# Kernel tuning notes

Hardware: AMD Instinct MI355X
Metric: run time of the kernel (lower is better)

Reference implementation:

```python
import jax, jax.numpy as jnp
import numpy as np

B, T, D, H = 2, 2048, 1024, 16
HD = D // H  # head_size = 64
EPS = 1e-5


def _layernorm(x, g, b):
    mu = jnp.mean(x, axis=-1, keepdims=True)
    var = jnp.mean(jnp.square(x - mu), axis=-1, keepdims=True)
    return (x - mu) * jax.lax.rsqrt(var + EPS) * g + b


def setup_inputs() -> dict:
    key = jax.random.key(0)
    ks = jax.random.split(key, 16)
    s = 0.02
    return {
        "x": jax.random.normal(ks[0], (B, T, D), jnp.float32),
        # per-head Q/K/V linears, stacked over heads: [H, D, HD] (in,out layout)
        "wq": jax.random.normal(ks[1], (H, D, HD), jnp.float32) * s,
        "bq": jnp.zeros((H, HD), jnp.float32),
        "wk": jax.random.normal(ks[2], (H, D, HD), jnp.float32) * s,
        "bk": jnp.zeros((H, HD), jnp.float32),
        "wv": jax.random.normal(ks[3], (H, D, HD), jnp.float32) * s,
        "bv": jnp.zeros((H, HD), jnp.float32),
        "wp": jax.random.normal(ks[4], (D, D), jnp.float32) * s,
        "bp": jnp.zeros((D,), jnp.float32),
        "w1": jax.random.normal(ks[5], (D, 4 * D), jnp.float32) * s,
        "b1": jnp.zeros((4 * D,), jnp.float32),
        "w2": jax.random.normal(ks[6], (4 * D, D), jnp.float32) * s,
        "b2": jnp.zeros((D,), jnp.float32),
        "ln1_g": jnp.ones((D,), jnp.float32),
        "ln1_b": jnp.zeros((D,), jnp.float32),
        "lnf_g": jnp.ones((D,), jnp.float32),
        "lnf_b": jnp.zeros((D,), jnp.float32),
        "ln2_g": jnp.ones((D,), jnp.float32),
        "ln2_b": jnp.zeros((D,), jnp.float32),
    }


def reference(x, wq, bq, wk, bk, wv, bv, wp, bp, w1, b1, w2, b2,
              ln1_g, ln1_b, lnf_g, lnf_b, ln2_g, ln2_b):
    b_, t_, d_ = x.shape
    # batched per-head projections: [B,H,T,HD]
    Q = jnp.einsum('btd,hde->bhte', x, wq) + bq[None, :, None, :]
    K = jnp.einsum('btd,hde->bhte', x, wk) + bk[None, :, None, :]
    V = jnp.einsum('btd,hde->bhte', x, wv) + bv[None, :, None, :]
    # raw attention scores, scaled -- NOTE: no softmax, no mask (matches source)
    wei = jnp.einsum('bhte,bhse->bhts', Q, K) * (HD ** -0.5)
    attn = jnp.einsum('bhts,bhse->bhte', wei, V)  # [B,H,T,HD]
    # concat heads along last dim == [B,T,H*HD]
    cat = attn.transpose(0, 2, 1, 3).reshape(b_, t_, d_)
    Kc = K.transpose(0, 2, 1, 3).reshape(b_, t_, d_)
    Vc = V.transpose(0, 2, 1, 3).reshape(b_, t_, d_)
    out = cat @ wp + bp
    out1 = _layernorm(x + out, ln1_g, ln1_b)
    # FeedForward: ln(idx + net(idx)) internally
    ff = jax.nn.relu(out1 @ w1 + b1) @ w2 + b2
    ffo = _layernorm(out1 + ff, lnf_g, lnf_b)
    out2 = _layernorm(out1 + ffo, ln2_g, ln2_b)
    return (out2, Kc, Vc)
```

## Files before the change

kernel.cpp:

```cpp
#include <hip/hip_runtime.h>

typedef unsigned short u16;
typedef __attribute__((ext_vector_type(4))) float f32x4;
typedef __attribute__((ext_vector_type(8))) __bf16 bf16x8;
typedef __attribute__((ext_vector_type(8))) unsigned short u16x8;
typedef __attribute__((ext_vector_type(4))) unsigned short u16x4;

__device__ __forceinline__ u16 f2b(float f) {
    unsigned int u = __builtin_bit_cast(unsigned int, f);
    u = (u + 0x7FFFu + ((u >> 16) & 1u)) >> 16;
    return (u16)u;
}
__device__ __forceinline__ float b2f(u16 h) {
    unsigned int u = ((unsigned int)h) << 16;
    return __builtin_bit_cast(float, u);
}

__device__ __forceinline__ void gload_lds16(const u16* g, u16* l) {
    __builtin_amdgcn_global_load_lds(
        (const __attribute__((address_space(1))) void*)g,
        (__attribute__((address_space(3))) void*)l,
        16, 0, 0);
}

__device__ __forceinline__ bf16x8 lds_frag(const u16* p) {
    u16x8 t = *(const u16x8*)p;
    return __builtin_bit_cast(bf16x8, t);
}

#define FENCE asm volatile("" ::: "memory")
#define BARRIER do { FENCE; __builtin_amdgcn_s_barrier(); FENCE; \
                     __builtin_amdgcn_sched_barrier(0); } while (0)
#define LGKM0 do { asm volatile("s_waitcnt lgkmcnt(0)" ::: "memory"); \
                   __builtin_amdgcn_sched_barrier(0); } while (0)
#define WAIT_VM8 do { asm volatile("s_waitcnt vmcnt(8)" ::: "memory"); \
                      __builtin_amdgcn_sched_barrier(0); } while (0)
#define WAIT_VM4 do { asm volatile("s_waitcnt vmcnt(4)" ::: "memory"); \
                      __builtin_amdgcn_sched_barrier(0); } while (0)
#define WAIT_VM0 do { asm volatile("s_waitcnt vmcnt(0)" ::: "memory"); \
                      __builtin_amdgcn_sched_barrier(0); } while (0)

__global__ __launch_bounds__(256) void cast_x_kernel(const float* __restrict__ in,
                                                     u16* __restrict__ out) {
    int i = (blockIdx.x * 256 + threadIdx.x) * 4;
    float4 v = *(const float4*)&in[i];
    u16x4 o = { f2b(v.x), f2b(v.y), f2b(v.z), f2b(v.w) };
    *(u16x4*)&out[i] = o;
}

__global__ __launch_bounds__(256) void tr_wqkv(const float* __restrict__ wq,
                                               const float* __restrict__ wk,
                                               const float* __restrict__ wv,
                                               u16* __restrict__ WT) {
    __shared__ float tile[32][33];
    int z = blockIdx.z;
    int sel = z >> 4, h = z & 15;
    const float* w = (sel == 0) ? wq : (sel == 1) ? wk : wv;
    w += (long)h * 65536;
    int tx = threadIdx.x & 31, ty = threadIdx.x >> 5;
    int d0 = blockIdx.x * 32, e0 = blockIdx.y * 32;
#pragma unroll
    for (int i = 0; i < 32; i += 8)
        tile[ty + i][tx] = w[(long)(d0 + ty + i) * 64 + e0 + tx];
    __syncthreads();
#pragma unroll
    for (int i = 0; i < 32; i += 8)
        WT[((long)(sel * 1024 + h * 64 + e0 + ty + i)) * 1024 + d0 + tx] = f2b(tile[tx][ty + i]);
}

__global__ __launch_bounds__(256) void prep_bias(const float* __restrict__ bq,
                                                 const float* __restrict__ bk,
                                                 const float* __restrict__ bv,
                                                 float* __restrict__ BI) {
    int i = blockIdx.x * 256 + threadIdx.x;
    const float* b = (i < 1024) ? bq : (i < 2048) ? bk : bv;
    BI[i] = b[((i & 1023) >> 6) * 64 + (i & 63)];
}

__global__ __launch_bounds__(256) void transpose_cast(const float* __restrict__ in,
                                                      u16* __restrict__ out, int R, int C) {
    __shared__ float tile[32][33];
    int tx = threadIdx.x & 31, ty = threadIdx.x >> 5;
    int r0 = blockIdx.y * 32, c0 = blockIdx.x * 32;
#pragma unroll
    for (int i = 0; i < 32; i += 8)
        tile[ty + i][tx] = in[(long)(r0 + ty + i) * C + c0 + tx];
    __syncthreads();
#pragma unroll
    for (int i = 0; i < 32; i += 8)
        out[(long)(c0 + ty + i) * R + r0 + tx] = f2b(tile[tx][ty + i]);
}

__global__ __launch_bounds__(256) void kv_expand(const u16* __restrict__ QKVB,
                                                 float* __restrict__ kv) {
    int idx = blockIdx.x * 256 + threadIdx.x;
    int row = idx >> 8;
    int co = (idx & 255) * 8;
    u16x8 v = *(const u16x8*)&QKVB[(long)row * 3072 + 1024 + co];
    float4 f0 = { b2f(v[0]), b2f(v[1]), b2f(v[2]), b2f(v[3]) };
    float4 f1 = { b2f(v[4]), b2f(v[5]), b2f(v[6]), b2f(v[7]) };
    long base = (long)(co >> 10) * 4194304 + (long)row * 1024 + (co & 1023);
    *(float4*)&kv[base] = f0;
    *(float4*)&kv[base + 4] = f1;
}

#define PHASEX(Sa, Sb, mh, kh, LOADB, STAGE_STMT, WAIT_STMT) do {             \
    if (LOADB) {                                                              \
        _Pragma("unroll") for (int n = 0; n < NF; ++n)                        \
            bfr[n] = lds_frag(&(Sb)[((brow0 + (n << 4)) << 6) +               \
                                    (eoff ^ ((kh) * 32))]);                   \
    }                                                                         \
    _Pragma("unroll") for (int m4 = 0; m4 < MFH; ++m4)                        \
        af[m4] = lds_frag(&(Sa)[((arow0 + (((mh) * MFH + m4) << 4)) << 6) +   \
                                (eoff ^ ((kh) * 32))]);                       \
    STAGE_STMT;                                                               \
    BARRIER;                                                                  \
    LGKM0;                                                                    \
    __builtin_amdgcn_s_setprio(1);                                            \
    _Pragma("unroll") for (int m4 = 0; m4 < MFH; ++m4)                        \
        _Pragma("unroll") for (int n = 0; n < NF; ++n)                        \
            acc[(mh) * MFH + m4][n] = __builtin_amdgcn_mfma_f32_16x16x32_bf16(\
                af[m4], bfr[n], acc[(mh) * MFH + m4][n], 0, 0, 0);            \
    __builtin_amdgcn_s_setprio(0);                                            \
    WAIT_STMT;                                                                \
    BARRIER;                                                                  \
} while (0)

template <int MODE, int WM, int WN, int MF, int NF, int MSPLIT>
__global__ __launch_bounds__(WM * WN * 64, 2) void gemmT(
    const u16* __restrict__ A, const u16* __restrict__ BT, const float* __restrict__ bias,
    u16* __restrict__ Cb, u16* __restrict__ Q0, u16* __restrict__ Q1,
    int M, int N, int K, int lda, int ldb, int ldc, int kchunk) {
    constexpr int T   = WM * WN * 64;
    constexpr int BM  = WM * MF * 16;
    constexpr int BN  = WN * NF * 16;
    constexpr int RPI = T / 8;
    constexpr int LA  = BM / RPI;
    constexpr int LB  = BN / RPI;
    constexpr int EPI = T * 8;
    constexpr int MFH = MF / MSPLIT;
    constexpr int ASZ = BM * 64, BSZ = BN * 64;
    __shared__ __align__(16) u16 SMEM[2 * ASZ + 2 * BSZ];
    u16* As0 = SMEM;
    u16* As1 = SMEM + ASZ;
    u16* Bs0 = SMEM + 2 * ASZ;
    u16* Bs1 = SMEM + 2 * ASZ + BSZ;
    const int tid = threadIdx.x;
    const int lane = tid & 63;
    const int wid = tid >> 6;
    const int wr = wid / WN, wc = wid % WN;
    const int ntile = N / BN;
    const int mtile = M / BM;
    int bid = blockIdx.x;
    int kb = 0, ksz = K;
    u16* Pout = Q0;
    if (MODE == 4) {
        int tiles = mtile * ntile;
        int sk = bid / tiles; bid -= sk * tiles;
        kb = sk * kchunk;
        int rem = K - kb; ksz = rem < kchunk ? rem : kchunk;
        Pout = sk ? Q1 : Q0;
    }
    {
        int q = (mtile * ntile) >> 3;
        bid = (bid & 7) * q + (bid >> 3);
    }
    const int bj = bid / mtile, bi = bid % mtile;
    const int brow = bi * BM, bcol = bj * BN;
    const int nt = ksz >> 6;
    const int niter = nt >> 1;

    const int srow = tid >> 3;
    const int scol = ((tid & 7) ^ (srow & 7)) << 3;
    const u16* ag = A + (long)(brow + srow) * lda + kb + scol;
    const u16* bg = BT + (long)(bcol + srow) * ldb + kb + scol;
    const long aI = (long)RPI * lda, bI = (long)RPI * ldb;
    const int sdst = tid << 3;

    auto STG = [&](u16* lA, u16* lB, int t, int half) {
#pragma unroll
        for (int j = 0; j < LA / 2; ++j)
            gload_lds16(ag + ((long)t << 6) + (half * (LA / 2) + j) * aI,
                        &lA[(half * (LA / 2) + j) * EPI + sdst]);
#pragma unroll
        for (int j = 0; j < LB / 2; ++j)
            gload_lds16(bg + ((long)t << 6) + (half * (LB / 2) + j) * bI,
                        &lB[(half * (LB / 2) + j) * EPI + sdst]);
    };

    f32x4 acc[MF][NF] = {};

    const int ln15 = lane & 15;
    const int eoff = (((lane >> 4) << 3) ^ ((lane & 7) << 3));
    const int arow0 = wr * (MF * 16) + ln15;
    const int brow0 = wc * (NF * 16) + ln15;

    STG(As0, Bs0, 0, 0); STG(As0, Bs0, 0, 1);
    if (nt > 1) { STG(As1, Bs1, 1, 0); STG(As1, Bs1, 1, 1); WAIT_VM8; }
    else WAIT_VM0;
    BARRIER;

    for (int I = 0; I < niter; ++I) {
        const int t0 = 2 * I;
        const bool hn0 = (t0 + 2 < nt);
        const bool hn1 = (t0 + 3 < nt);
        const bool notlast = (I + 1 < niter);
        bf16x8 af[MFH], bfr[NF];
        if constexpr (MSPLIT == 2) {
            PHASEX(As0, Bs0, 0, 0, true,  { if (I > 0) STG(As1, Bs1, t0 + 1, 1); }, {});
            PHASEX(As0, Bs0, 1, 0, false, {}, {});
            PHASEX(As0, Bs0, 0, 1, true,  {}, {});
            PHASEX(As0, Bs0, 1, 1, false, { if (hn0) STG(As0, Bs0, t0 + 2, 0); },
                   { if (hn0) WAIT_VM4; else WAIT_VM0; });
            PHASEX(As1, Bs1, 0, 0, true,  { if (hn0) STG(As0, Bs0, t0 + 2, 1); }, {});
            PHASEX(As1, Bs1, 1, 0, false, {}, {});
            PHASEX(As1, Bs1, 0, 1, true,  {}, {});
            PHASEX(As1, Bs1, 1, 1, false, { if (hn1) STG(As1, Bs1, t0 + 3, 0); },
                   { if (notlast) { if (hn1) WAIT_VM4; else WAIT_VM0; } });
        } else {
            PHASEX(As0, Bs0, 0, 0, true,  { if (I > 0) STG(As1, Bs1, t0 + 1, 1); }, {});
            PHASEX(As0, Bs0, 0, 1, true,  { if (hn0) STG(As0, Bs0, t0 + 2, 0); },
                   { if (hn0) WAIT_VM4; else WAIT_VM0; });
            PHASEX(As1, Bs1, 0, 0, true,  { if (hn0) STG(As0, Bs0, t0 + 2, 1); }, {});
            PHASEX(As1, Bs1, 0, 1, true,  { if (hn1) STG(As1, Bs1, t0 + 3, 0); },
                   { if (notlast) { if (hn1) WAIT_VM4; else WAIT_VM0; } });
        }
    }

    const int crow0 = wr * (MF * 16), ccol0 = wc * (NF * 16);
#pragma unroll
    for (int m = 0; m < MF; ++m) {
        int rbase = crow0 + (m << 4) + ((lane >> 4) << 2);
#pragma unroll
        for (int n = 0; n < NF; ++n) {
            int col = ccol0 + (n << 4) + ln15;
            float bv = (MODE == 4) ? 0.f : bias[bcol + col];
#pragma unroll
            for (int r = 0; r < 4; ++r) {
                float v = acc[m][n][r] + bv;
                if (MODE == 2) v = v > 0.f ? v : 0.f;
                SMEM[(rbase + r) * BN + col] = f2b(v);
            }
        }
    }
    LGKM0;
    BARRIER;
    u16* outp = (MODE == 4) ? Pout : Cb;
    constexpr int CHT = BM * BN / 8 / T;
#pragma unroll
    for (int k = 0; k < CHT; ++k) {
        int c = tid + k * T;
        int row = c / (BN / 8), co = (c % (BN / 8)) * 8;
        u16x8 vv = *(const u16x8*)&SMEM[row * BN + co];
        *(u16x8*)&outp[(long)(brow + row) * ldc + bcol + co] = vv;
    }
}

__global__ __launch_bounds__(256) void ktv_partial(const u16* __restrict__ QKVB,
                                                   float* __restrict__ KTVF) {
    __shared__ __align__(16) u16 Ks[64 * 64];
    __shared__ __align__(16) u16 Vs[64 * 64];
    int tid = threadIdx.x;
    int tc = blockIdx.x, bh = blockIdx.y;
    int b = bh >> 4, h = bh & 15;
    int j = tid & 63, i0 = (tid >> 6) * 16;
    float acc[16] = {};
    for (int st = 0; st < 4; ++st) {
        int t0 = tc * 256 + st * 64;
        __syncthreads();
#pragma unroll
        for (int i = 0; i < 2; ++i) {
            int c = i * 256 + tid;
            long base = (long)(b * 2048 + t0 + (c >> 3)) * 3072 + h * 64 + (c & 7) * 8;
            *(u16x8*)&Ks[c * 8] = *(const u16x8*)&QKVB[base + 1024];
            *(u16x8*)&Vs[c * 8] = *(const u16x8*)&QKVB[base + 2048];
        }
        __syncthreads();
        for (int tt = 0; tt < 64; ++tt) {
            float vj = b2f(Vs[tt * 64 + j]);
            u16x8 k0 = *(const u16x8*)&Ks[tt * 64 + i0];
            u16x8 k1 = *(const u16x8*)&Ks[tt * 64 + i0 + 8];
#pragma unroll
            for (int r = 0; r < 8; ++r) acc[r] += b2f(k0[r]) * vj;
#pragma unroll
            for (int r = 0; r < 8; ++r) acc[r + 8] += b2f(k1[r]) * vj;
        }
    }
#pragma unroll
    for (int r = 0; r < 16; ++r)
        atomicAdd(&KTVF[bh * 4096 + (i0 + r) * 64 + j], acc[r]);
}

__global__ __launch_bounds__(256) void cast_ktv(const float* __restrict__ KTVF,
                                                u16* __restrict__ KTVT) {
    int idx = blockIdx.x * 256 + threadIdx.x;
    int bh = idx >> 12, r = idx & 4095;
    int n = r >> 6, k = r & 63;
    KTVT[idx] = f2b(KTVF[bh * 4096 + k * 64 + n] * 0.125f);
}

__global__ __launch_bounds__(256) void attn_gemm(const u16* __restrict__ QKVB,
                                                 const u16* __restrict__ KTVT,
                                                 u16* __restrict__ cat) {
    __shared__ __align__(16) u16 Qs[64 * 64];
    __shared__ __align__(16) u16 Bs[64 * 64];
    int tid = threadIdx.x, wid = tid >> 6, lane = tid & 63;
    int rt = blockIdx.x, bh = blockIdx.y;
    int b = bh >> 4, h = bh & 15;
    long qbase = (long)(b * 2048 + rt * 64) * 3072 + h * 64;
#pragma unroll
    for (int i = 0; i < 2; ++i) {
        int c = i * 256 + tid;
        gload_lds16(QKVB + qbase + (c >> 3) * 3072 + (c & 7) * 8, &Qs[(i * 256 + wid * 64) * 8]);
        gload_lds16(KTVT + bh * 4096 + c * 8, &Bs[(i * 256 + wid * 64) * 8]);
    }
    __syncthreads();
    f32x4 acc[4] = {};
#pragma unroll
    for (int kk = 0; kk < 2; ++kk) {
        bf16x8 a = lds_frag(&Qs[(wid * 16 + (lane & 15)) * 64 + kk * 32 + (lane >> 4) * 8]);
#pragma unroll
        for (int n = 0; n < 4; ++n) {
            bf16x8 bb = lds_frag(&Bs[(n * 16 + (lane & 15)) * 64 + kk * 32 + (lane >> 4) * 8]);
            acc[n] = __builtin_amdgcn_mfma_f32_16x16x32_bf16(a, bb, acc[n], 0, 0, 0);
        }
    }
#pragma unroll
    for (int n = 0; n < 4; ++n)
#pragma unroll
        for (int r = 0; r < 4; ++r) {
            int row = rt * 64 + wid * 16 + (lane >> 4) * 4 + r;
            int col = h * 64 + n * 16 + (lane & 15);
            cat[(long)(b * 2048 + row) * 1024 + col] = f2b(acc[n][r]);
        }
}

__device__ __forceinline__ void block_reduce2(float& a, float& b) {
    __syncthreads();
#pragma unroll
    for (int off = 32; off; off >>= 1) {
        a += __shfl_down(a, off);
        b += __shfl_down(b, off);
    }
    __shared__ float sa[4], sb[4];
    int wid = threadIdx.x >> 6, lane = threadIdx.x & 63;
    if (lane == 0) { sa[wid] = a; sb[wid] = b; }
    __syncthreads();
    a = sa[0] + sa[1] + sa[2] + sa[3];
    b = sb[0] + sb[1] + sb[2] + sb[3];
}

__global__ __launch_bounds__(256) void ln1_kernel(
    const float* __restrict__ x,
    const u16* __restrict__ q0, const u16* __restrict__ q1,
    const float* __restrict__ bp,
    const float* __restrict__ g, const float* __restrict__ bt,
    float* __restrict__ out1f, u16* __restrict__ out1b) {
    int row = blockIdx.x, tid = threadIdx.x;
    long base = (long)row * 1024 + tid * 4;
    float4 xv = *(const float4*)&x[base];
    u16x4 a0 = *(const u16x4*)&q0[base];
    u16x4 a1 = *(const u16x4*)&q1[base];
    float4 bb = *(const float4*)&bp[tid * 4];
    float xa[4] = { xv.x, xv.y, xv.z, xv.w };
    float bba[4] = { bb.x, bb.y, bb.z, bb.w };
    float s[4];
#pragma unroll
    for (int r = 0; r < 4; ++r)
        s[r] = xa[r] + b2f(a0[r]) + b2f(a1[r]) + bba[r];
    float sum = s[0] + s[1] + s[2] + s[3];
    float sq = s[0] * s[0] + s[1] * s[1] + s[2] * s[2] + s[3] * s[3];
    block_reduce2(sum, sq);
    float mu = sum * (1.f / 1024.f);
    float var = sq * (1.f / 1024.f) - mu * mu;
    float rs = rsqrtf(var + 1e-5f);
    float o0 = (s[0] - mu) * rs * g[tid * 4 + 0] + bt[tid * 4 + 0];
    float o1 = (s[1] - mu) * rs * g[tid * 4 + 1] + bt[tid * 4 + 1];
    float o2 = (s[2] - mu) * rs * g[tid * 4 + 2] + bt[tid * 4 + 2];
    float o3 = (s[3] - mu) * rs * g[tid * 4 + 3] + bt[tid * 4 + 3];
    float4 of; of.x = o0; of.y = o1; of.z = o2; of.w = o3;
    u16x4 ob = (u16x4){ f2b(o0), f2b(o1), f2b(o2), f2b(o3) };
    *(float4*)&out1f[base] = of;
    *(u16x4*)&out1b[base] = ob;
}

__global__ __launch_bounds__(256) void lnf_kernel(
    const float* __restrict__ out1f,
    const u16* __restrict__ q0, const u16* __restrict__ q1,
    const float* __restrict__ b2,
    const float* __restrict__ lnfg, const float* __restrict__ lnfb,
    const float* __restrict__ ln2g, const float* __restrict__ ln2b,
    float* __restrict__ out2) {
    int row = blockIdx.x, tid = threadIdx.x;
    long base = (long)row * 1024 + tid * 4;
    float4 o1 = *(const float4*)&out1f[base];
    u16x4 a0 = *(const u16x4*)&q0[base];
    u16x4 a1 = *(const u16x4*)&q1[base];
    float4 bb = *(const float4*)&b2[tid * 4];
    float o1a[4] = { o1.x, o1.y, o1.z, o1.w };
    float bba[4] = { bb.x, bb.y, bb.z, bb.w };
    float s1[4];
#pragma unroll
    for (int r = 0; r < 4; ++r)
        s1[r] = o1a[r] + b2f(a0[r]) + b2f(a1[r]) + bba[r];
    float sum = s1[0] + s1[1] + s1[2] + s1[3];
    float sq = s1[0] * s1[0] + s1[1] * s1[1] + s1[2] * s1[2] + s1[3] * s1[3];
    block_reduce2(sum, sq);
    float mu = sum * (1.f / 1024.f);
    float rs = rsqrtf(sq * (1.f / 1024.f) - mu * mu + 1e-5f);
    float s2[4];
#pragma unroll
    for (int r = 0; r < 4; ++r) {
        float ffo = (s1[r] - mu) * rs * lnfg[tid * 4 + r] + lnfb[tid * 4 + r];
        s2[r] = o1a[r] + ffo;
    }
    float sum2 = s2[0] + s2[1] + s2[2] + s2[3];
    float sq2 = s2[0] * s2[0] + s2[1] * s2[1] + s2[2] * s2[2] + s2[3] * s2[3];
    block_reduce2(sum2, sq2);
    float mu2 = sum2 * (1.f / 1024.f);
    float rs2 = rsqrtf(sq2 * (1.f / 1024.f) - mu2 * mu2 + 1e-5f);
    float4 o;
    o.x = (s2[0] - mu2) * rs2 * ln2g[tid * 4 + 0] + ln2b[tid * 4 + 0];
    o.y = (s2[1] - mu2) * rs2 * ln2g[tid * 4 + 1] + ln2b[tid * 4 + 1];
    o.z = (s2[2] - mu2) * rs2 * ln2g[tid * 4 + 2] + ln2b[tid * 4 + 2];
    o.w = (s2[3] - mu2) * rs2 * ln2g[tid * 4 + 3] + ln2b[tid * 4 + 3];
    *(float4*)&out2[base] = o;
}

extern "C" void kernel_launch(void* const* d_in, const int* in_sizes, int n_in,
                              void* d_out, int out_size, void* d_ws, size_t ws_size,
                              hipStream_t stream) {
    const float* x    = (const float*)d_in[0];
    const float* wq   = (const float*)d_in[1];
    const float* bq   = (const float*)d_in[2];
    const float* wk   = (const float*)d_in[3];
    const float* bk   = (const float*)d_in[4];
    const float* wv   = (const float*)d_in[5];
    const float* bv   = (const float*)d_in[6];
    const float* wp   = (const float*)d_in[7];
    const float* bp   = (const float*)d_in[8];
    const float* w1   = (const float*)d_in[9];
    const float* b1   = (const float*)d_in[10];
    const float* w2   = (const float*)d_in[11];
    const float* b2   = (const float*)d_in[12];
    const float* ln1g = (const float*)d_in[13];
    const float* ln1b = (const float*)d_in[14];
    const float* lnfg = (const float*)d_in[15];
    const float* lnfb = (const float*)d_in[16];
    const float* ln2g = (const float*)d_in[17];
    const float* ln2b = (const float*)d_in[18];

    float* out2 = (float*)d_out;
    float* kv   = (float*)d_out + 4194304;

    char* ws = (char*)d_ws;
    u16*   XB     = (u16*)  (ws + 0);
    u16*   CAT    = XB;
    u16*   WQKVT  = (u16*)  (ws + 8388608);
    float* BQKV   = (float*)(ws + 14680064);
    u16*   WPT    = (u16*)  (ws + 14692352);
    u16*   W1T    = (u16*)  (ws + 16789504);
    u16*   W2T    = (u16*)  (ws + 25178112);
    float* KTVF   = (float*)(ws + 33566720);
    u16*   KTVT   = (u16*)  (ws + 34091008);
    u16*   QKVB   = (u16*)  (ws + 34353152);
    u16*   OUT1B  = QKVB;
    u16*   Q3_0   = (u16*)  (ws + 59518976);
    u16*   Q3_1   = (u16*)  (ws + 67907584);
    float* OUT1F  = (float*)(ws + 76296192);
    u16*   H1     = (u16*)  (ws + 93073408);
    u16*   Q5_0   = (u16*)  (ws + 0);
    u16*   Q5_1   = (u16*)  (ws + 34353152);
    (void)ws_size; (void)in_sizes; (void)n_in; (void)out_size;

    hipMemsetAsync(KTVF, 0, 32 * 4096 * 4, stream);
    cast_x_kernel<<<4096, 256, 0, stream>>>(x, XB);
    tr_wqkv<<<dim3(32, 2, 48), 256, 0, stream>>>(wq, wk, wv, WQKVT);
    prep_bias<<<12, 256, 0, stream>>>(bq, bk, bv, BQKV);
    transpose_cast<<<dim3(32, 32), 256, 0, stream>>>(wp, WPT, 1024, 1024);
    transpose_cast<<<dim3(128, 32), 256, 0, stream>>>(w1, W1T, 1024, 4096);
    transpose_cast<<<dim3(32, 128), 256, 0, stream>>>(w2, W2T, 4096, 1024);

    gemmT<1, 2, 4, 4, 6, 2><<<256, 512, 0, stream>>>(
        XB, WQKVT, BQKV, QKVB, nullptr, nullptr,
        4096, 3072, 1024, 1024, 1024, 3072, 0);
    kv_expand<<<4096, 256, 0, stream>>>(QKVB, kv);
    ktv_partial<<<dim3(8, 32), 256, 0, stream>>>(QKVB, KTVF);
    cast_ktv<<<512, 256, 0, stream>>>(KTVF, KTVT);
    attn_gemm<<<dim3(32, 32), 256, 0, stream>>>(QKVB, KTVT, CAT);

    gemmT<4, 2, 2, 4, 4, 1><<<512, 256, 0, stream>>>(
        CAT, WPT, nullptr, nullptr, Q3_0, Q3_1,
        4096, 1024, 1024, 1024, 1024, 1024, 512);
    ln1_kernel<<<4096, 256, 0, stream>>>(x, Q3_0, Q3_1, bp, ln1g, ln1b, OUT1F, OUT1B);

    gemmT<2, 2, 4, 8, 4, 2><<<256, 512, 0, stream>>>(
        OUT1B, W1T, b1, H1, nullptr, nullptr,
        4096, 4096, 1024, 1024, 1024, 4096, 0);
    gemmT<4, 2, 2, 4, 4, 1><<<512, 256, 0, stream>>>(
        H1, W2T, nullptr, nullptr, Q5_0, Q5_1,
        4096, 1024, 4096, 4096, 4096, 1024, 2048);
    lnf_kernel<<<4096, 256, 0, stream>>>(OUT1F, Q5_0, Q5_1, b2,
                                         lnfg, lnfb, ln2g, ln2b, out2);
}
```

Baseline: 220.5 us.

## Rewrite GEMM main loop with register double-buffered fragments and swizzled epilogue

```diff
diff --git a/kernel.cpp b/kernel.cpp
--- a/kernel.cpp
+++ b/kernel.cpp
@@ -31,11 +31,10 @@
 #define FENCE asm volatile("" ::: "memory")
 #define BARRIER do { FENCE; __builtin_amdgcn_s_barrier(); FENCE; \
                      __builtin_amdgcn_sched_barrier(0); } while (0)
+#define SCHED0 __builtin_amdgcn_sched_barrier(0)
 #define LGKM0 do { asm volatile("s_waitcnt lgkmcnt(0)" ::: "memory"); \
                    __builtin_amdgcn_sched_barrier(0); } while (0)
 #define WAIT_VM8 do { asm volatile("s_waitcnt vmcnt(8)" ::: "memory"); \
-                      __builtin_amdgcn_sched_barrier(0); } while (0)
-#define WAIT_VM4 do { asm volatile("s_waitcnt vmcnt(4)" ::: "memory"); \
                       __builtin_amdgcn_sched_barrier(0); } while (0)
 #define WAIT_VM0 do { asm volatile("s_waitcnt vmcnt(0)" ::: "memory"); \
                       __builtin_amdgcn_sched_barrier(0); } while (0)
@@ -104,29 +103,7 @@
     *(float4*)&kv[base + 4] = f1;
 }
 
-#define PHASEX(Sa, Sb, mh, kh, LOADB, STAGE_STMT, WAIT_STMT) do {             \
-    if (LOADB) {                                                              \
-        _Pragma("unroll") for (int n = 0; n < NF; ++n)                        \
-            bfr[n] = lds_frag(&(Sb)[((brow0 + (n << 4)) << 6) +               \
-                                    (eoff ^ ((kh) * 32))]);                   \
-    }                                                                         \
-    _Pragma("unroll") for (int m4 = 0; m4 < MFH; ++m4)                        \
-        af[m4] = lds_frag(&(Sa)[((arow0 + (((mh) * MFH + m4) << 4)) << 6) +   \
-                                (eoff ^ ((kh) * 32))]);                       \
-    STAGE_STMT;                                                               \
-    BARRIER;                                                                  \
-    LGKM0;                                                                    \
-    __builtin_amdgcn_s_setprio(1);                                            \
-    _Pragma("unroll") for (int m4 = 0; m4 < MFH; ++m4)                        \
-        _Pragma("unroll") for (int n = 0; n < NF; ++n)                        \
-            acc[(mh) * MFH + m4][n] = __builtin_amdgcn_mfma_f32_16x16x32_bf16(\
-                af[m4], bfr[n], acc[(mh) * MFH + m4][n], 0, 0, 0);            \
-    __builtin_amdgcn_s_setprio(0);                                            \
-    WAIT_STMT;                                                                \
-    BARRIER;                                                                  \
-} while (0)
-
-template <int MODE, int WM, int WN, int MF, int NF, int MSPLIT>
+template <int MODE, int WM, int WN, int MF, int NF, bool COLOUT>
 __global__ __launch_bounds__(WM * WN * 64, 2) void gemmT(
     const u16* __restrict__ A, const u16* __restrict__ BT, const float* __restrict__ bias,
     u16* __restrict__ Cb, u16* __restrict__ Q0, u16* __restrict__ Q1,
@@ -138,7 +115,7 @@
     constexpr int LA  = BM / RPI;
     constexpr int LB  = BN / RPI;
     constexpr int EPI = T * 8;
-    constexpr int MFH = MF / MSPLIT;
+    constexpr int MFH = MF / 2;
     constexpr int ASZ = BM * 64, BSZ = BN * 64;
     __shared__ __align__(16) u16 SMEM[2 * ASZ + 2 * BSZ];
     u16* As0 = SMEM;
@@ -165,10 +142,11 @@
         int q = (mtile * ntile) >> 3;
         bid = (bid & 7) * q + (bid >> 3);
     }
-    const int bj = bid / mtile, bi = bid % mtile;
+    int bi, bj;
+    if (COLOUT) { bj = bid / mtile; bi = bid % mtile; }
+    else        { bi = bid / ntile; bj = bid % ntile; }
     const int brow = bi * BM, bcol = bj * BN;
     const int nt = ksz >> 6;
-    const int niter = nt >> 1;
 
     const int srow = tid >> 3;
     const int scol = ((tid & 7) ^ (srow & 7)) << 3;
@@ -177,54 +155,68 @@
     const long aI = (long)RPI * lda, bI = (long)RPI * ldb;
     const int sdst = tid << 3;
 
-    auto STG = [&](u16* lA, u16* lB, int t, int half) {
-#pragma unroll
-        for (int j = 0; j < LA / 2; ++j)
-            gload_lds16(ag + ((long)t << 6) + (half * (LA / 2) + j) * aI,
-                        &lA[(half * (LA / 2) + j) * EPI + sdst]);
-#pragma unroll
-        for (int j = 0; j < LB / 2; ++j)
-            gload_lds16(bg + ((long)t << 6) + (half * (LB / 2) + j) * bI,
-                        &lB[(half * (LB / 2) + j) * EPI + sdst]);
+    auto STAGE = [&](u16* lA, u16* lB, int t) {
+#pragma unroll
+        for (int j = 0; j < LA; ++j)
+            gload_lds16(ag + ((long)t << 6) + j * aI, &lA[j * EPI + sdst]);
+#pragma unroll
+        for (int j = 0; j < LB; ++j)
+            gload_lds16(bg + ((long)t << 6) + j * bI, &lB[j * EPI + sdst]);
     };
 
     f32x4 acc[MF][NF] = {};
+    bf16x8 af0[MFH], af1[MFH], bf0[NF], bf1[NF];
 
     const int ln15 = lane & 15;
     const int eoff = (((lane >> 4) << 3) ^ ((lane & 7) << 3));
     const int arow0 = wr * (MF * 16) + ln15;
     const int brow0 = wc * (NF * 16) + ln15;
 
-    STG(As0, Bs0, 0, 0); STG(As0, Bs0, 0, 1);
-    if (nt > 1) { STG(As1, Bs1, 1, 0); STG(As1, Bs1, 1, 1); WAIT_VM8; }
-    else WAIT_VM0;
+#define RD_A(dst, S, kh, mh)                                                   \
+    _Pragma("unroll") for (int m4 = 0; m4 < MFH; ++m4)                         \
+        dst[m4] = lds_frag(&(S)[((arow0 + (((mh) * MFH + m4) << 4)) << 6) +    \
+                                (eoff ^ ((kh) << 5))]);
+#define RD_B(dst, S, kh)                                                       \
+    _Pragma("unroll") for (int n = 0; n < NF; ++n)                             \
+        dst[n] = lds_frag(&(S)[((brow0 + (n << 4)) << 6) + (eoff ^ ((kh) << 5))]);
+#define MM(a, b, mh) do {                                                      \
+    __builtin_amdgcn_s_setprio(1);                                             \
+    _Pragma("unroll") for (int m4 = 0; m4 < MFH; ++m4)                         \
+        _Pragma("unroll") for (int n = 0; n < NF; ++n)                         \
+            acc[(mh) * MFH + m4][n] = __builtin_amdgcn_mfma_f32_16x16x32_bf16( \
+                a[m4], b[n], acc[(mh) * MFH + m4][n], 0, 0, 0);                \
+    __builtin_amdgcn_s_setprio(0);                                             \
+} while (0)
+
+    STAGE(As0, Bs0, 0);
+    if (nt > 1) { STAGE(As1, Bs1, 1); WAIT_VM8; } else { WAIT_VM0; }
     BARRIER;
-
-    for (int I = 0; I < niter; ++I) {
-        const int t0 = 2 * I;
-        const bool hn0 = (t0 + 2 < nt);
-        const bool hn1 = (t0 + 3 < nt);
-        const bool notlast = (I + 1 < niter);
-        bf16x8 af[MFH], bfr[NF];
-        if constexpr (MSPLIT == 2) {
-            PHASEX(As0, Bs0, 0, 0, true,  { if (I > 0) STG(As1, Bs1, t0 + 1, 1); }, {});
-            PHASEX(As0, Bs0, 1, 0, false, {}, {});
-            PHASEX(As0, Bs0, 0, 1, true,  {}, {});
-            PHASEX(As0, Bs0, 1, 1, false, { if (hn0) STG(As0, Bs0, t0 + 2, 0); },
-                   { if (hn0) WAIT_VM4; else WAIT_VM0; });
-            PHASEX(As1, Bs1, 0, 0, true,  { if (hn0) STG(As0, Bs0, t0 + 2, 1); }, {});
-            PHASEX(As1, Bs1, 1, 0, false, {}, {});
-            PHASEX(As1, Bs1, 0, 1, true,  {}, {});
-            PHASEX(As1, Bs1, 1, 1, false, { if (hn1) STG(As1, Bs1, t0 + 3, 0); },
-                   { if (notlast) { if (hn1) WAIT_VM4; else WAIT_VM0; } });
-        } else {
-            PHASEX(As0, Bs0, 0, 0, true,  { if (I > 0) STG(As1, Bs1, t0 + 1, 1); }, {});
-            PHASEX(As0, Bs0, 0, 1, true,  { if (hn0) STG(As0, Bs0, t0 + 2, 0); },
-                   { if (hn0) WAIT_VM4; else WAIT_VM0; });
-            PHASEX(As1, Bs1, 0, 0, true,  { if (hn0) STG(As0, Bs0, t0 + 2, 1); }, {});
-            PHASEX(As1, Bs1, 0, 1, true,  { if (hn1) STG(As1, Bs1, t0 + 3, 0); },
-                   { if (notlast) { if (hn1) WAIT_VM4; else WAIT_VM0; } });
-        }
+    RD_B(bf0, Bs0, 0);
+    RD_A(af0, As0, 0, 0);
+
+    u16 *Ac = As0, *Bc = Bs0, *Ao = As1, *Bo = Bs1;
+    for (int t = 0; t < nt; ++t) {
+        const bool hasN = (t + 1 < nt);
+        const bool hasNN = (t + 2 < nt);
+        RD_A(af1, Ac, 0, 1);
+        MM(af0, bf0, 0);
+        SCHED0;
+        RD_B(bf1, Bc, 1);
+        RD_A(af0, Ac, 1, 0);
+        MM(af1, bf0, 1);
+        SCHED0;
+        RD_A(af1, Ac, 1, 1);
+        MM(af0, bf1, 0);
+        WAIT_VM0;
+        BARRIER;
+        if (hasN) { RD_B(bf0, Bo, 0); RD_A(af0, Ao, 0, 0); }
+        MM(af1, bf1, 1);
+        BARRIER;
+        if (hasNN) STAGE(Ac, Bc, t + 2);
+        SCHED0;
+        u16* tp;
+        tp = Ac; Ac = Ao; Ao = tp;
+        tp = Bc; Bc = Bo; Bo = tp;
     }
 
     const int crow0 = wr * (MF * 16), ccol0 = wc * (NF * 16);
@@ -239,7 +231,8 @@
             for (int r = 0; r < 4; ++r) {
                 float v = acc[m][n][r] + bv;
                 if (MODE == 2) v = v > 0.f ? v : 0.f;
-                SMEM[(rbase + r) * BN + col] = f2b(v);
+                int row = rbase + r;
+                SMEM[row * BN + (col ^ ((row & 7) << 3))] = f2b(v);
             }
         }
     }
@@ -251,9 +244,12 @@
     for (int k = 0; k < CHT; ++k) {
         int c = tid + k * T;
         int row = c / (BN / 8), co = (c % (BN / 8)) * 8;
-        u16x8 vv = *(const u16x8*)&SMEM[row * BN + co];
+        u16x8 vv = *(const u16x8*)&SMEM[row * BN + (co ^ ((row & 7) << 3))];
         *(u16x8*)&outp[(long)(brow + row) * ldc + bcol + co] = vv;
     }
+#undef RD_A
+#undef RD_B
+#undef MM
 }
 
 __global__ __launch_bounds__(256) void ktv_partial(const u16* __restrict__ QKVB,
@@ -481,7 +477,7 @@
     transpose_cast<<<dim3(128, 32), 256, 0, stream>>>(w1, W1T, 1024, 4096);
     transpose_cast<<<dim3(32, 128), 256, 0, stream>>>(w2, W2T, 4096, 1024);
 
-    gemmT<1, 2, 4, 4, 6, 2><<<256, 512, 0, stream>>>(
+    gemmT<1, 2, 4, 4, 6, true><<<256, 512, 0, stream>>>(
         XB, WQKVT, BQKV, QKVB, nullptr, nullptr,
         4096, 3072, 1024, 1024, 1024, 3072, 0);
     kv_expand<<<4096, 256, 0, stream>>>(QKVB, kv);
@@ -489,15 +485,15 @@
     cast_ktv<<<512, 256, 0, stream>>>(KTVF, KTVT);
     attn_gemm<<<dim3(32, 32), 256, 0, stream>>>(QKVB, KTVT, CAT);
 
-    gemmT<4, 2, 2, 4, 4, 1><<<512, 256, 0, stream>>>(
+    gemmT<4, 2, 2, 4, 4, false><<<512, 256, 0, stream>>>(
         CAT, WPT, nullptr, nullptr, Q3_0, Q3_1,
         4096, 1024, 1024, 1024, 1024, 1024, 512);
     ln1_kernel<<<4096, 256, 0, stream>>>(x, Q3_0, Q3_1, bp, ln1g, ln1b, OUT1F, OUT1B);
 
-    gemmT<2, 2, 4, 8, 4, 2><<<256, 512, 0, stream>>>(
+    gemmT<2, 2, 4, 8, 4, false><<<256, 512, 0, stream>>>(
         OUT1B, W1T, b1, H1, nullptr, nullptr,
         4096, 4096, 1024, 1024, 1024, 4096, 0);
-    gemmT<4, 2, 2, 4, 4, 1><<<512, 256, 0, stream>>>(
+    gemmT<4, 2, 2, 4, 4, false><<<512, 256, 0, stream>>>(
         H1, W2T, nullptr, nullptr, Q5_0, Q5_1,
         4096, 1024, 4096, 4096, 4096, 1024, 2048);
     lnf_kernel<<<4096, 256, 0, stream>>>(OUT1F, Q5_0, Q5_1, b2,
```

Result: faster. 209.6 us (-5.0%).
